# Kernel tuning notes

Hardware: AMD Instinct MI355X
Metric: run time of the kernel (lower is better)

Reference implementation:

```python
import jax, jax.numpy as jnp
import numpy as np

N_NODES = 90  # hard-coded per-graph node count in the original module
HIDDEN = 128


def setup_inputs() -> dict:
    key = jax.random.key(0)
    ks = jax.random.split(key, 12)
    B = 8192
    adj = jax.random.uniform(ks[0], (B, N_NODES, N_NODES), dtype=jnp.float32)
    s_in = 1.0 / np.sqrt(N_NODES)
    s_h = 1.0 / np.sqrt(HIDDEN)
    return {
        "adj": adj,
        "W_mlp0": jax.random.normal(ks[1], (N_NODES, HIDDEN), jnp.float32) * s_in,
        "b_mlp0": jax.random.normal(ks[2], (HIDDEN,), jnp.float32) * s_in,
        "W_mlp1": jax.random.normal(ks[3], (HIDDEN, HIDDEN), jnp.float32) * s_h,
        "b_mlp1": jax.random.normal(ks[4], (HIDDEN,), jnp.float32) * s_h,
        "W_mlp2": jax.random.normal(ks[5], (HIDDEN, HIDDEN), jnp.float32) * s_h,
        "b_mlp2": jax.random.normal(ks[6], (HIDDEN,), jnp.float32) * s_h,
        "W_res1": jax.random.normal(ks[7], (HIDDEN, HIDDEN), jnp.float32) * s_h,
        "b_res1": jax.random.normal(ks[8], (HIDDEN,), jnp.float32) * s_h,
        "W_res2": jax.random.normal(ks[9], (HIDDEN, HIDDEN), jnp.float32) * s_h,
        "b_res2": jax.random.normal(ks[10], (HIDDEN,), jnp.float32) * s_h,
    }


def reference(adj, W_mlp0, b_mlp0, W_mlp1, b_mlp1, W_mlp2, b_mlp2,
              W_res1, b_res1, W_res2, b_res2):
    B = adj.shape[0]
    # raw node features: identity per graph (torch.eye(90) concatenated)
    raw_x = jnp.broadcast_to(jnp.eye(N_NODES, dtype=adj.dtype), (B, N_NODES, N_NODES))

    def gconv(x, W, b):
        # block-diagonal Adj_block @ x == batched per-graph matmul, then linear
        return jnp.einsum('bij,bjk->bik', adj, x) @ W + b

    # encoding == 1 branch, layers = 3
    h0 = gconv(raw_x, W_mlp0, b_mlp0)                    # mlps[0](raw_x, A)
    r1 = h0 @ W_res1 + b_res1                            # res[1](h0)
    x = jax.nn.relu(gconv(h0, W_mlp1, b_mlp1)) + r1      # layer 1
    Y = jax.nn.relu(gconv(x, W_mlp2, b_mlp2) + (r1 @ W_res2 + b_res2))  # final

    # decoder: per-graph inner-product, concatenated along node axis
    Z = jnp.einsum('bik,bjk->bij', Y, Y)                 # [B, 90, 90]
    return Z.reshape(B * N_NODES, N_NODES)
```

## Files before the change

kernel.cpp:

```cpp
#include <hip/hip_runtime.h>


#define NN 90
#define HH 128
#define NT 256

typedef _Float16 half8 __attribute__((ext_vector_type(8)));
typedef _Float16 half2v __attribute__((ext_vector_type(2)));
typedef float floatx16 __attribute__((ext_vector_type(16)));
typedef unsigned int uint4v __attribute__((ext_vector_type(4)));

#define AST 104
#define AST8 13
#define ASTU 52
#define SR 136
#define SR8 17

#define MFMA(a, b, c) __builtin_amdgcn_mfma_f32_32x32x16_f16((a), (b), (c), 0, 0, 0)

__global__ void prep_stage1(const float* __restrict__ W0,
                            const float* __restrict__ Wr1,
                            const float* __restrict__ b0,
                            const float* __restrict__ br1,
                            float* __restrict__ WdF,
                            float* __restrict__ c1F)
{
    const int idx = blockIdx.x * blockDim.x + threadIdx.x;
    if (idx < NN * HH) {
        const int k = idx >> 7, nn = idx & 127;
        float s = 0.f;
        for (int q = 0; q < HH; q++) s += W0[k * HH + q] * Wr1[q * HH + nn];
        WdF[idx] = s;
    } else if (idx < NN * HH + HH) {
        const int nn = idx - NN * HH;
        float s = br1[nn];
        for (int q = 0; q < HH; q++) s += b0[q] * Wr1[q * HH + nn];
        c1F[nn] = s;
    }
}

__global__ void prep_stage2(const float* __restrict__ W0,
                            const float* __restrict__ W1,
                            const float* __restrict__ W2,
                            const float* __restrict__ Wr2,
                            const float* __restrict__ b2,
                            const float* __restrict__ br2,
                            const float* __restrict__ WdF,
                            const float* __restrict__ c1F,
                            _Float16* __restrict__ ws)
{
    const int idx = blockIdx.x * blockDim.x + threadIdx.x;
    if (idx < 12288) {
        const int nn = idx / 96, k = idx - nn * 96;
        ws[idx] = (k < NN) ? (_Float16)W0[k * HH + nn] : (_Float16)0.f;
    } else if (idx < 24576) {
        const int j = idx - 12288;
        const int nn = j / 96, k = j - nn * 96;
        _Float16 v = (_Float16)0.f;
        if (k < NN)       v = (_Float16)WdF[k * HH + nn];
        else if (k == NN) v = (_Float16)c1F[nn];
        ws[idx] = v;
    } else if (idx < 36864) {
        const int j = idx - 24576;
        const int nn = j / 96, k = j - nn * 96;
        _Float16 v = (_Float16)0.f;
        if (k < NN) {
            float s = 0.f;
            for (int q = 0; q < HH; q++) s += WdF[k * HH + q] * Wr2[q * HH + nn];
            v = (_Float16)s;
        } else if (k == NN) {
            float s = b2[nn] + br2[nn];
            for (int q = 0; q < HH; q++) s += c1F[q] * Wr2[q * HH + nn];
            v = (_Float16)s;
        }
        ws[idx] = v;
    } else if (idx < 53248) {
        const int j = idx - 36864;
        const int nn = j >> 7, k = j & 127;
        ws[idx] = (_Float16)W1[k * HH + nn];
    } else if (idx < 69632) {
        const int j = idx - 53248;
        const int nn = j >> 7, k = j & 127;
        ws[idx] = (_Float16)W2[k * HH + nn];
    }
}

__global__ __launch_bounds__(NT, 3) void graphcnn_mfma(
    const float* __restrict__ adj,
    const _Float16* __restrict__ wts,
    const float* __restrict__ b0, const float* __restrict__ b1,
    float* __restrict__ out)
{
    __shared__ __align__(16) unsigned char smem[46080];
    _Float16* adjH = (_Float16*)smem;
    _Float16* B1   = (_Float16*)(smem + 19968);

    const int t    = threadIdx.x;
    const int wv   = t >> 6;
    const int lane = t & 63;
    const int p    = lane & 31;
    const int h    = lane >> 5;
    const int n    = wv * 32 + p;

    const _Float16* W0T = wts;
    const _Float16* WdT = wts + 12288;
    const _Float16* WeT = wts + 24576;
    const _Float16* W1T = wts + 36864;
    const _Float16* W2T = wts + 53248;

    {
        const float* Ag = adj + (size_t)blockIdx.x * (NN * NN);
        unsigned* aH = (unsigned*)adjH;
        #pragma unroll
        for (int it = 0; it < 18; it++) {
            const int i = t + it * NT;
            const int r = i / 48, cc = i - r * 48;
            unsigned val = 0u;
            if (r < NN && cc < 45) {
                const float2 v = *(const float2*)(Ag + r * NN + cc * 2);
                const half2v hv = { (_Float16)v.x, (_Float16)v.y };
                val = __builtin_bit_cast(unsigned, hv);
            }
            aH[r * ASTU + cc] = val;
        }
    }

    auto writeR = [&](_Float16* buf, const floatx16& A0, const floatx16& A1,
                      const floatx16& A2) {
        #pragma unroll
        for (int mt = 0; mt < 3; mt++) {
            const floatx16& A = (mt == 0) ? A0 : (mt == 1) ? A1 : A2;
            #pragma unroll
            for (int r = 0; r < 16; r++) {
                const int node = mt * 32 + (r & 3) + 8 * (r >> 2) + 4 * h;
                buf[node * SR + n] = (_Float16)A[r];
            }
        }
    };

    uint4v frg[6];
    auto buildFrags = [&](const floatx16& A0, const floatx16& A1, const floatx16& A2) {
        #pragma unroll
        for (int mt = 0; mt < 3; mt++) {
            const floatx16& A = (mt == 0) ? A0 : (mt == 1) ? A1 : A2;
            #pragma unroll
            for (int s01 = 0; s01 < 2; s01++) {
                const int s = 8 * s01;
                const half2v x0 = { (_Float16)A[s + 0], (_Float16)A[s + 1] };
                const half2v x1 = { (_Float16)A[s + 2], (_Float16)A[s + 3] };
                const half2v y0 = { (_Float16)A[s + 4], (_Float16)A[s + 5] };
                const half2v y1 = { (_Float16)A[s + 6], (_Float16)A[s + 7] };
                const unsigned X0 = __builtin_bit_cast(unsigned, x0);
                const unsigned X1 = __builtin_bit_cast(unsigned, x1);
                const unsigned Y0 = __builtin_bit_cast(unsigned, y0);
                const unsigned Y1 = __builtin_bit_cast(unsigned, y1);
                const unsigned R0 = __shfl_xor(h ? X0 : Y0, 32, 64);
                const unsigned R1 = __shfl_xor(h ? X1 : Y1, 32, 64);
                uint4v f;
                f[0] = h ? R0 : X0;
                f[1] = h ? R1 : X1;
                f[2] = h ? Y0 : R0;
                f[3] = h ? Y1 : R1;
                frg[mt * 2 + s01] = f;
            }
        }
    };

    __syncthreads();

    floatx16 acc0, acc1, acc2;

    {
        half8 bw[6];
        #pragma unroll
        for (int kt = 0; kt < 6; kt++) bw[kt] = ((const half8*)W0T)[n * 12 + kt * 2 + h];
        const float bias = b0[n];
        #pragma unroll
        for (int r = 0; r < 16; r++) { acc0[r] = bias; acc1[r] = bias; acc2[r] = bias; }
        #pragma unroll
        for (int kt = 0; kt < 6; kt++) {
            const half8 a0 = ((const half8*)adjH)[(0 * 32 + p) * AST8 + kt * 2 + h];
            const half8 a1 = ((const half8*)adjH)[(1 * 32 + p) * AST8 + kt * 2 + h];
            const half8 a2 = ((const half8*)adjH)[(2 * 32 + p) * AST8 + kt * 2 + h];
            acc0 = MFMA(a0, bw[kt], acc0);
            acc1 = MFMA(a1, bw[kt], acc1);
            acc2 = MFMA(a2, bw[kt], acc2);
        }
        buildFrags(acc0, acc1, acc2);
    }

    {
        #pragma unroll
        for (int r = 0; r < 16; r++) { acc0[r] = 0.f; acc1[r] = 0.f; acc2[r] = 0.f; }
        #pragma unroll
        for (int kt = 0; kt < 6; kt++) {
            const half8 bfk = __builtin_bit_cast(half8, frg[kt]);
            const half8 a0 = ((const half8*)adjH)[(0 * 32 + p) * AST8 + kt * 2 + h];
            const half8 a1 = ((const half8*)adjH)[(1 * 32 + p) * AST8 + kt * 2 + h];
            const half8 a2 = ((const half8*)adjH)[(2 * 32 + p) * AST8 + kt * 2 + h];
            acc0 = MFMA(a0, bfk, acc0);
            acc1 = MFMA(a1, bfk, acc1);
            acc2 = MFMA(a2, bfk, acc2);
        }
        writeR(B1, acc0, acc1, acc2);
    }

    half8 r1p[6];
    {
        half8 bw[6];
        #pragma unroll
        for (int kt = 0; kt < 6; kt++) bw[kt] = ((const half8*)WdT)[n * 12 + kt * 2 + h];
        const float bias = (float)WdT[n * 96 + 90];
        floatx16 ra, rb, rc;
        #pragma unroll
        for (int r = 0; r < 16; r++) { ra[r] = bias; rb[r] = bias; rc[r] = bias; }
        #pragma unroll
        for (int kt = 0; kt < 6; kt++) {
            const half8 a0 = ((const half8*)adjH)[(0 * 32 + p) * AST8 + kt * 2 + h];
            const half8 a1 = ((const half8*)adjH)[(1 * 32 + p) * AST8 + kt * 2 + h];
            const half8 a2 = ((const half8*)adjH)[(2 * 32 + p) * AST8 + kt * 2 + h];
            ra = MFMA(a0, bw[kt], ra);
            rb = MFMA(a1, bw[kt], rb);
            rc = MFMA(a2, bw[kt], rc);
        }
        #pragma unroll
        for (int mt = 0; mt < 3; mt++) {
            const floatx16& A = (mt == 0) ? ra : (mt == 1) ? rb : rc;
            #pragma unroll
            for (int s01 = 0; s01 < 2; s01++) {
                half8 v;
                #pragma unroll
                for (int j = 0; j < 8; j++) v[j] = (_Float16)A[8 * s01 + j];
                r1p[mt * 2 + s01] = v;
            }
        }
    }
    __syncthreads();

    {
        half8 bw[8];
        #pragma unroll
        for (int kt = 0; kt < 8; kt++) bw[kt] = ((const half8*)W1T)[n * 16 + kt * 2 + h];
        const float bias = b1[n];
        #pragma unroll
        for (int r = 0; r < 16; r++) { acc0[r] = bias; acc1[r] = bias; acc2[r] = bias; }
        #pragma unroll
        for (int kt = 0; kt < 8; kt++) {
            const half8 a0 = ((const half8*)B1)[(0 * 32 + p) * SR8 + kt * 2 + h];
            const half8 a1 = ((const half8*)B1)[(1 * 32 + p) * SR8 + kt * 2 + h];
            const half8 a2 = ((const half8*)B1)[(2 * 32 + p) * SR8 + kt * 2 + h];
            acc0 = MFMA(a0, bw[kt], acc0);
            acc1 = MFMA(a1, bw[kt], acc1);
            acc2 = MFMA(a2, bw[kt], acc2);
        }
        #pragma unroll
        for (int r = 0; r < 16; r++) {
            acc0[r] = fmaxf(acc0[r], 0.f) + (float)r1p[0 * 2 + (r >> 3)][r & 7];
            acc1[r] = fmaxf(acc1[r], 0.f) + (float)r1p[1 * 2 + (r >> 3)][r & 7];
            acc2[r] = fmaxf(acc2[r], 0.f) + (float)r1p[2 * 2 + (r >> 3)][r & 7];
        }
        buildFrags(acc0, acc1, acc2);
    }
    __syncthreads();

    {
        #pragma unroll
        for (int r = 0; r < 16; r++) { acc0[r] = 0.f; acc1[r] = 0.f; acc2[r] = 0.f; }
        #pragma unroll
        for (int kt = 0; kt < 6; kt++) {
            const half8 bfk = __builtin_bit_cast(half8, frg[kt]);
            const half8 a0 = ((const half8*)adjH)[(0 * 32 + p) * AST8 + kt * 2 + h];
            const half8 a1 = ((const half8*)adjH)[(1 * 32 + p) * AST8 + kt * 2 + h];
            const half8 a2 = ((const half8*)adjH)[(2 * 32 + p) * AST8 + kt * 2 + h];
            acc0 = MFMA(a0, bfk, acc0);
            acc1 = MFMA(a1, bfk, acc1);
            acc2 = MFMA(a2, bfk, acc2);
        }
        writeR(B1, acc0, acc1, acc2);
    }
    __syncthreads();

    {
        half8 bw[8];
        #pragma unroll
        for (int kt = 0; kt < 8; kt++) bw[kt] = ((const half8*)W2T)[n * 16 + kt * 2 + h];
        const float bias = (float)WeT[n * 96 + 90];
        #pragma unroll
        for (int r = 0; r < 16; r++) { acc0[r] = bias; acc1[r] = bias; acc2[r] = bias; }
        #pragma unroll
        for (int kt = 0; kt < 8; kt++) {
            const half8 a0 = ((const half8*)B1)[(0 * 32 + p) * SR8 + kt * 2 + h];
            const half8 a1 = ((const half8*)B1)[(1 * 32 + p) * SR8 + kt * 2 + h];
            const half8 a2 = ((const half8*)B1)[(2 * 32 + p) * SR8 + kt * 2 + h];
            acc0 = MFMA(a0, bw[kt], acc0);
            acc1 = MFMA(a1, bw[kt], acc1);
            acc2 = MFMA(a2, bw[kt], acc2);
        }
        half8 bg[6];
        #pragma unroll
        for (int kt = 0; kt < 6; kt++) bg[kt] = ((const half8*)WeT)[n * 12 + kt * 2 + h];
        #pragma unroll
        for (int kt = 0; kt < 6; kt++) {
            const half8 a0 = ((const half8*)adjH)[(0 * 32 + p) * AST8 + kt * 2 + h];
            const half8 a1 = ((const half8*)adjH)[(1 * 32 + p) * AST8 + kt * 2 + h];
            const half8 a2 = ((const half8*)adjH)[(2 * 32 + p) * AST8 + kt * 2 + h];
            acc0 = MFMA(a0, bg[kt], acc0);
            acc1 = MFMA(a1, bg[kt], acc1);
            acc2 = MFMA(a2, bg[kt], acc2);
        }
    }
    __syncthreads();
    {
        _Float16* YR = B1;
        #pragma unroll
        for (int mt = 0; mt < 3; mt++) {
            const floatx16& A = (mt == 0) ? acc0 : (mt == 1) ? acc1 : acc2;
            #pragma unroll
            for (int r = 0; r < 16; r++) {
                const int node = mt * 32 + (r & 3) + 8 * (r >> 2) + 4 * h;
                YR[node * SR + n] = (_Float16)fmaxf(A[r], 0.f);
            }
        }
    }
    __syncthreads();

    {
        const _Float16* YR = B1;
        float* outb = out + (size_t)blockIdx.x * (NN * NN);
        auto ztile = [&](int mt, int nt) {
            floatx16 acc;
            #pragma unroll
            for (int r = 0; r < 16; r++) acc[r] = 0.f;
            #pragma unroll
            for (int kt = 0; kt < 8; kt++) {
                const half8 av = ((const half8*)YR)[(mt * 32 + p) * SR8 + kt * 2 + h];
                const half8 bv = ((const half8*)YR)[(nt * 32 + p) * SR8 + kt * 2 + h];
                acc = MFMA(av, bv, acc);
            }
            const int col = nt * 32 + p;
            if (col < NN) {
                #pragma unroll
                for (int r = 0; r < 16; r++) {
                    const int row = mt * 32 + (r & 3) + 8 * (r >> 2) + 4 * h;
                    if (row < NN) outb[row * NN + col] = acc[r];
                }
            }
        };
        if      (wv == 0) { ztile(0, 0); ztile(0, 1); ztile(0, 2); }
        else if (wv == 1) { ztile(1, 0); ztile(1, 1); }
        else if (wv == 2) { ztile(1, 2); ztile(2, 0); }
        else              { ztile(2, 1); ztile(2, 2); }
    }
}

extern "C" void kernel_launch(void* const* d_in, const int* in_sizes, int n_in,
                              void* d_out, int out_size, void* d_ws, size_t ws_size,
                              hipStream_t stream) {
    const float* adj = (const float*)d_in[0];
    const float* W0  = (const float*)d_in[1];
    const float* b0  = (const float*)d_in[2];
    const float* W1  = (const float*)d_in[3];
    const float* b1  = (const float*)d_in[4];
    const float* W2  = (const float*)d_in[5];
    const float* b2  = (const float*)d_in[6];
    const float* Wr1 = (const float*)d_in[7];
    const float* br1 = (const float*)d_in[8];
    const float* Wr2 = (const float*)d_in[9];
    const float* br2 = (const float*)d_in[10];
    float* out = (float*)d_out;
    _Float16* wts = (_Float16*)d_ws;

    float* WdF = (float*)((char*)d_ws + 139264);
    float* c1F = (float*)((char*)d_ws + 185344);

    prep_stage1<<<12, 1024, 0, stream>>>(W0, Wr1, b0, br1, WdF, c1F);
    prep_stage2<<<68, 1024, 0, stream>>>(W0, W1, W2, Wr2, b2, br2, WdF, c1F, wts);

    const int B = in_sizes[0] / (NN * NN);
    graphcnn_mfma<<<B, NT, 0, stream>>>(adj, wts, b0, b1, out);
}
```

Measured before the change: 681.0 us.

## Compact and XOR-swizzle shared memory buffers, raise occupancy to four blocks

Replaces the padded shared-memory layouts for the fp16 adjacency and intermediate feature buffers with unpadded, XOR-swizzled layouts. The adjacency is split into two column regions, and rows past 89 are clamped instead of stored as zeros. This shrinks LDS per block from 46080 to 40320 bytes so launch bounds can ask for four blocks per CU. The swizzle is meant to avoid bank conflicts without padding, at the cost of extra index arithmetic and possible register pressure under the tighter occupancy bound.

```diff
diff --git a/kernel.cpp b/kernel.cpp
--- a/kernel.cpp
+++ b/kernel.cpp
@@ -9,12 +9,6 @@
 typedef _Float16 half2v __attribute__((ext_vector_type(2)));
 typedef float floatx16 __attribute__((ext_vector_type(16)));
 typedef unsigned int uint4v __attribute__((ext_vector_type(4)));
-
-#define AST 104
-#define AST8 13
-#define ASTU 52
-#define SR 136
-#define SR8 17
 
 #define MFMA(a, b, c) __builtin_amdgcn_mfma_f32_32x32x16_f16((a), (b), (c), 0, 0, 0)
 
@@ -85,15 +79,16 @@
     }
 }
 
-__global__ __launch_bounds__(NT, 3) void graphcnn_mfma(
+__global__ __launch_bounds__(NT, 4) void graphcnn_mfma(
     const float* __restrict__ adj,
     const _Float16* __restrict__ wts,
     const float* __restrict__ b0, const float* __restrict__ b1,
     float* __restrict__ out)
 {
-    __shared__ __align__(16) unsigned char smem[46080];
-    _Float16* adjH = (_Float16*)smem;
-    _Float16* B1   = (_Float16*)(smem + 19968);
+    __shared__ __align__(16) unsigned char smem[40320];
+    _Float16* adj1 = (_Float16*)smem;
+    _Float16* adj2 = (_Float16*)(smem + 11520);
+    _Float16* B1   = (_Float16*)(smem + 17280);
 
     const int t    = threadIdx.x;
     const int wv   = t >> 6;
@@ -108,41 +103,61 @@
     const _Float16* W1T = wts + 36864;
     const _Float16* W2T = wts + 53248;
 
+    const int r0 = p;
+    const int r1 = 32 + p;
+    const int r2 = (64 + p > 89) ? 89 : (64 + p);
+
     {
         const float* Ag = adj + (size_t)blockIdx.x * (NN * NN);
-        unsigned* aH = (unsigned*)adjH;
-        #pragma unroll
-        for (int it = 0; it < 18; it++) {
+        unsigned* a1u = (unsigned*)adj1;
+        unsigned* a2u = (unsigned*)adj2;
+        #pragma unroll
+        for (int it = 0; it < 17; it++) {
             const int i = t + it * NT;
-            const int r = i / 48, cc = i - r * 48;
-            unsigned val = 0u;
-            if (r < NN && cc < 45) {
-                const float2 v = *(const float2*)(Ag + r * NN + cc * 2);
-                const half2v hv = { (_Float16)v.x, (_Float16)v.y };
-                val = __builtin_bit_cast(unsigned, hv);
-            }
-            aH[r * ASTU + cc] = val;
-        }
-    }
-
-    auto writeR = [&](_Float16* buf, const floatx16& A0, const floatx16& A1,
-                      const floatx16& A2) {
+            if (i < 4320) {
+                const int r = i / 48, cc = i - r * 48;
+                unsigned val = 0u;
+                if (cc < 45) {
+                    const float2 v = *(const float2*)(Ag + r * NN + cc * 2);
+                    const half2v hv = { (_Float16)v.x, (_Float16)v.y };
+                    val = __builtin_bit_cast(unsigned, hv);
+                }
+                if (cc < 32) a1u[r * 32 + (cc ^ ((r & 7) << 2))] = val;
+                else         a2u[r * 16 + ((cc - 32) ^ ((r & 3) << 2))] = val;
+            }
+        }
+    }
+
+    auto rdA = [&](int row, int kt) -> half8 {
+        if (kt < 4)
+            return ((const half8*)adj1)[row * 8 + (((kt * 2 + h)) ^ (row & 7))];
+        else
+            return ((const half8*)adj2)[row * 4 + (((kt - 4) * 2 + h) ^ (row & 3))];
+    };
+    auto rdB = [&](int row, int kt) -> half8 {
+        return ((const half8*)B1)[row * 16 + ((kt * 2 + h) ^ (row & 7))];
+    };
+
+    auto writeR = [&](const floatx16& A0, const floatx16& A1f,
+                      const floatx16& A2f) {
         #pragma unroll
         for (int mt = 0; mt < 3; mt++) {
-            const floatx16& A = (mt == 0) ? A0 : (mt == 1) ? A1 : A2;
+            const floatx16& A = (mt == 0) ? A0 : (mt == 1) ? A1f : A2f;
             #pragma unroll
             for (int r = 0; r < 16; r++) {
                 const int node = mt * 32 + (r & 3) + 8 * (r >> 2) + 4 * h;
-                buf[node * SR + n] = (_Float16)A[r];
+                if (node < NN)
+                    B1[node * 128 + (n ^ ((node & 7) << 3))] = (_Float16)A[r];
             }
         }
     };
 
     uint4v frg[6];
-    auto buildFrags = [&](const floatx16& A0, const floatx16& A1, const floatx16& A2) {
+    auto buildFrags = [&](const floatx16& A0, const floatx16& A1f,
+                          const floatx16& A2f) {
         #pragma unroll
         for (int mt = 0; mt < 3; mt++) {
-            const floatx16& A = (mt == 0) ? A0 : (mt == 1) ? A1 : A2;
+            const floatx16& A = (mt == 0) ? A0 : (mt == 1) ? A1f : A2f;
             #pragma unroll
             for (int s01 = 0; s01 < 2; s01++) {
                 const int s = 8 * s01;
@@ -179,12 +194,9 @@
         for (int r = 0; r < 16; r++) { acc0[r] = bias; acc1[r] = bias; acc2[r] = bias; }
         #pragma unroll
         for (int kt = 0; kt < 6; kt++) {
-            const half8 a0 = ((const half8*)adjH)[(0 * 32 + p) * AST8 + kt * 2 + h];
-            const half8 a1 = ((const half8*)adjH)[(1 * 32 + p) * AST8 + kt * 2 + h];
-            const half8 a2 = ((const half8*)adjH)[(2 * 32 + p) * AST8 + kt * 2 + h];
-            acc0 = MFMA(a0, bw[kt], acc0);
-            acc1 = MFMA(a1, bw[kt], acc1);
-            acc2 = MFMA(a2, bw[kt], acc2);
+            acc0 = MFMA(rdA(r0, kt), bw[kt], acc0);
+            acc1 = MFMA(rdA(r1, kt), bw[kt], acc1);
+            acc2 = MFMA(rdA(r2, kt), bw[kt], acc2);
         }
         buildFrags(acc0, acc1, acc2);
     }
@@ -195,14 +207,11 @@
         #pragma unroll
         for (int kt = 0; kt < 6; kt++) {
             const half8 bfk = __builtin_bit_cast(half8, frg[kt]);
-            const half8 a0 = ((const half8*)adjH)[(0 * 32 + p) * AST8 + kt * 2 + h];
-            const half8 a1 = ((const half8*)adjH)[(1 * 32 + p) * AST8 + kt * 2 + h];
-            const half8 a2 = ((const half8*)adjH)[(2 * 32 + p) * AST8 + kt * 2 + h];
-            acc0 = MFMA(a0, bfk, acc0);
-            acc1 = MFMA(a1, bfk, acc1);
-            acc2 = MFMA(a2, bfk, acc2);
-        }
-        writeR(B1, acc0, acc1, acc2);
+            acc0 = MFMA(rdA(r0, kt), bfk, acc0);
+            acc1 = MFMA(rdA(r1, kt), bfk, acc1);
+            acc2 = MFMA(rdA(r2, kt), bfk, acc2);
+        }
+        writeR(acc0, acc1, acc2);
     }
 
     half8 r1p[6];
@@ -216,12 +225,9 @@
         for (int r = 0; r < 16; r++) { ra[r] = bias; rb[r] = bias; rc[r] = bias; }
         #pragma unroll
         for (int kt = 0; kt < 6; kt++) {
-            const half8 a0 = ((const half8*)adjH)[(0 * 32 + p) * AST8 + kt * 2 + h];
-            const half8 a1 = ((const half8*)adjH)[(1 * 32 + p) * AST8 + kt * 2 + h];
-            const half8 a2 = ((const half8*)adjH)[(2 * 32 + p) * AST8 + kt * 2 + h];
-            ra = MFMA(a0, bw[kt], ra);
-            rb = MFMA(a1, bw[kt], rb);
-            rc = MFMA(a2, bw[kt], rc);
+            ra = MFMA(rdA(r0, kt), bw[kt], ra);
+            rb = MFMA(rdA(r1, kt), bw[kt], rb);
+            rc = MFMA(rdA(r2, kt), bw[kt], rc);
         }
         #pragma unroll
         for (int mt = 0; mt < 3; mt++) {
@@ -246,12 +252,9 @@
         for (int r = 0; r < 16; r++) { acc0[r] = bias; acc1[r] = bias; acc2[r] = bias; }
         #pragma unroll
         for (int kt = 0; kt < 8; kt++) {
-            const half8 a0 = ((const half8*)B1)[(0 * 32 + p) * SR8 + kt * 2 + h];
-            const half8 a1 = ((const half8*)B1)[(1 * 32 + p) * SR8 + kt * 2 + h];
-            const half8 a2 = ((const half8*)B1)[(2 * 32 + p) * SR8 + kt * 2 + h];
-            acc0 = MFMA(a0, bw[kt], acc0);
-            acc1 = MFMA(a1, bw[kt], acc1);
-            acc2 = MFMA(a2, bw[kt], acc2);
+            acc0 = MFMA(rdB(r0, kt), bw[kt], acc0);
+            acc1 = MFMA(rdB(r1, kt), bw[kt], acc1);
+            acc2 = MFMA(rdB(r2, kt), bw[kt], acc2);
         }
         #pragma unroll
         for (int r = 0; r < 16; r++) {
@@ -269,14 +272,11 @@
         #pragma unroll
         for (int kt = 0; kt < 6; kt++) {
             const half8 bfk = __builtin_bit_cast(half8, frg[kt]);
-            const half8 a0 = ((const half8*)adjH)[(0 * 32 + p) * AST8 + kt * 2 + h];
-            const half8 a1 = ((const half8*)adjH)[(1 * 32 + p) * AST8 + kt * 2 + h];
-            const half8 a2 = ((const half8*)adjH)[(2 * 32 + p) * AST8 + kt * 2 + h];
-            acc0 = MFMA(a0, bfk, acc0);
-            acc1 = MFMA(a1, bfk, acc1);
-            acc2 = MFMA(a2, bfk, acc2);
-        }
-        writeR(B1, acc0, acc1, acc2);
+            acc0 = MFMA(rdA(r0, kt), bfk, acc0);
+            acc1 = MFMA(rdA(r1, kt), bfk, acc1);
+            acc2 = MFMA(rdA(r2, kt), bfk, acc2);
+        }
+        writeR(acc0, acc1, acc2);
     }
     __syncthreads();
 
@@ -289,53 +289,47 @@
         for (int r = 0; r < 16; r++) { acc0[r] = bias; acc1[r] = bias; acc2[r] = bias; }
         #pragma unroll
         for (int kt = 0; kt < 8; kt++) {
-            const half8 a0 = ((const half8*)B1)[(0 * 32 + p) * SR8 + kt * 2 + h];
-            const half8 a1 = ((const half8*)B1)[(1 * 32 + p) * SR8 + kt * 2 + h];
-            const half8 a2 = ((const half8*)B1)[(2 * 32 + p) * SR8 + kt * 2 + h];
-            acc0 = MFMA(a0, bw[kt], acc0);
-            acc1 = MFMA(a1, bw[kt], acc1);
-            acc2 = MFMA(a2, bw[kt], acc2);
+            acc0 = MFMA(rdB(r0, kt), bw[kt], acc0);
+            acc1 = MFMA(rdB(r1, kt), bw[kt], acc1);
+            acc2 = MFMA(rdB(r2, kt), bw[kt], acc2);
         }
         half8 bg[6];
         #pragma unroll
         for (int kt = 0; kt < 6; kt++) bg[kt] = ((const half8*)WeT)[n * 12 + kt * 2 + h];
         #pragma unroll
         for (int kt = 0; kt < 6; kt++) {
-            const half8 a0 = ((const half8*)adjH)[(0 * 32 + p) * AST8 + kt * 2 + h];
-            const half8 a1 = ((const half8*)adjH)[(1 * 32 + p) * AST8 + kt * 2 + h];
-            const half8 a2 = ((const half8*)adjH)[(2 * 32 + p) * AST8 + kt * 2 + h];
-            acc0 = MFMA(a0, bg[kt], acc0);
-            acc1 = MFMA(a1, bg[kt], acc1);
-            acc2 = MFMA(a2, bg[kt], acc2);
-        }
-    }
-    __syncthreads();
-    {
-        _Float16* YR = B1;
+            acc0 = MFMA(rdA(r0, kt), bg[kt], acc0);
+            acc1 = MFMA(rdA(r1, kt), bg[kt], acc1);
+            acc2 = MFMA(rdA(r2, kt), bg[kt], acc2);
+        }
+    }
+    __syncthreads();
+    {
         #pragma unroll
         for (int mt = 0; mt < 3; mt++) {
             const floatx16& A = (mt == 0) ? acc0 : (mt == 1) ? acc1 : acc2;
             #pragma unroll
             for (int r = 0; r < 16; r++) {
                 const int node = mt * 32 + (r & 3) + 8 * (r >> 2) + 4 * h;
-                YR[node * SR + n] = (_Float16)fmaxf(A[r], 0.f);
-            }
-        }
-    }
-    __syncthreads();
-
-    {
-        const _Float16* YR = B1;
+                if (node < NN)
+                    B1[node * 128 + (n ^ ((node & 7) << 3))] = (_Float16)fmaxf(A[r], 0.f);
+            }
+        }
+    }
+    __syncthreads();
+
+    {
         float* outb = out + (size_t)blockIdx.x * (NN * NN);
+        const int q0 = r0, q1 = r1, q2 = r2;
         auto ztile = [&](int mt, int nt) {
+            const int ra_ = (mt == 0) ? q0 : (mt == 1) ? q1 : q2;
+            const int rb_ = (nt == 0) ? q0 : (nt == 1) ? q1 : q2;
             floatx16 acc;
             #pragma unroll
             for (int r = 0; r < 16; r++) acc[r] = 0.f;
             #pragma unroll
             for (int kt = 0; kt < 8; kt++) {
-                const half8 av = ((const half8*)YR)[(mt * 32 + p) * SR8 + kt * 2 + h];
-                const half8 bv = ((const half8*)YR)[(nt * 32 + p) * SR8 + kt * 2 + h];
-                acc = MFMA(av, bv, acc);
+                acc = MFMA(rdB(ra_, kt), rdB(rb_, kt), acc);
             }
             const int col = nt * 32 + p;
             if (col < NN) {
```

Measured after the change: 1.116 ms. 1.64x slower.
